# Kernel optimization log

Hardware: AMD Instinct MI355X
Metric: run time of the kernel (lower is better)

The kernel has to match this reference:

```python
import jax, jax.numpy as jnp
import numpy as np

C, H, W = 3, 32, 32
DIM = C * H * W
NUM_CLUSTERS = 4096
BATCH = 8192


def setup_inputs() -> dict:
    key = jax.random.key(0)
    k_x, k_t, k_m = jax.random.split(key, 3)
    x = jax.random.normal(k_x, (BATCH, C, H, W), dtype=jnp.float32)
    t = jax.random.uniform(k_t, (1,), dtype=jnp.float32)
    means = jax.random.normal(k_m, (NUM_CLUSTERS, C, H, W), dtype=jnp.float32)
    # normalize each cluster mean to unit L2 norm over (C,H,W), as in __init__
    norms = jnp.sqrt(jnp.sum(means ** 2, axis=(1, 2, 3), keepdims=True))
    means = means / norms
    standard_dev = jnp.ones((1,), dtype=jnp.float32)  # sqrt(init_variance=1.0)
    return {"x": x, "t": t, "means": means, "standard_dev": standard_dev}


def reference(x, t, means, standard_dev):
    B = x.shape[0]
    x_f = x.reshape(B, -1)                      # [B, D]
    scale = jnp.exp(-t)                         # [1]
    variance = 1.0 - scale ** 2                 # [1]
    variance_t = scale ** 2 * standard_dev ** 2 + variance  # [1]

    sc = means.reshape(means.shape[0], -1) * scale          # [N, D] scaled clusters

    x_sq = jnp.sum(x_f ** 2, axis=-1, keepdims=True)        # [B, 1]
    c_sq = jnp.sum(sc ** 2, axis=-1)[None, :]               # [1, N]
    d2 = jnp.maximum(x_sq + c_sq - 2.0 * (x_f @ sc.T), 0.0)  # [B, N]

    weights = -0.5 * d2 / variance_t                        # [B, N]
    normalized_weights = jax.nn.softmax(weights, axis=-1)   # [B, N]

    cluster_term = normalized_weights @ sc                  # [B, D]

    denoiser_weight = scale ** 2 * standard_dev ** 2 / variance_t  # [1]
    out = denoiser_weight * x_f + (1.0 - denoiser_weight) * cluster_term
    out = out / scale
    return out.reshape(B, C, H, W)
```

## Files before the change

kernel.cpp:

```cpp
#include <hip/hip_runtime.h>
#include <hip/hip_bf16.h>
#include <math.h>
#include <stdint.h>

#define BATCH 8192
#define NCLUST 4096
#define DIM 3072

typedef __bf16 bf16;
typedef __bf16 bf16x4 __attribute__((ext_vector_type(4)));
typedef __bf16 bf16x8 __attribute__((ext_vector_type(8)));
typedef float f32x4 __attribute__((ext_vector_type(4)));

__device__ __forceinline__ void get_scalars(const float* t, const float* sdv,
                                            float& scale, float& vt, float& dw) {
    float s = expf(-t[0]);
    float sd = sdv[0];
    float s2sd2 = s * s * sd * sd;
    float var = 1.0f - s * s;
    scale = s;
    vt = s2sd2 + var;
    dw = s2sd2 / vt;
}

__device__ __forceinline__ void async16(const bf16* g, bf16* l) {
    __builtin_amdgcn_global_load_lds(
        (const __attribute__((address_space(1))) void*)g,
        (__attribute__((address_space(3))) void*)l, 16, 0, 0);
}


__global__ __launch_bounds__(256) void cvt_x_kernel(const float* __restrict__ x,
                                                    bf16* __restrict__ xb, int n4) {
    int i = blockIdx.x * blockDim.x + threadIdx.x;
    if (i >= n4) return;
    float4 v = ((const float4*)x)[i];
    bf16x4 o = {(bf16)v.x, (bf16)v.y, (bf16)v.z, (bf16)v.w};
    ((bf16x4*)xb)[i] = o;
}

__global__ __launch_bounds__(256) void prep_sc_kernel(const float* __restrict__ means,
                                                      const float* __restrict__ t,
                                                      bf16* __restrict__ scb,
                                                      float* __restrict__ c_sq) {
    __shared__ float red[4];
    int row = blockIdx.x, tid = threadIdx.x;
    float scale = expf(-t[0]);
    const float4* m4 = (const float4*)(means + (size_t)row * DIM);
    bf16x4* o4 = (bf16x4*)(scb + (size_t)row * DIM);
    float s = 0.f;
#pragma unroll
    for (int j = 0; j < 3; ++j) {
        float4 v = m4[tid + 256 * j];
        float a = v.x * scale, b = v.y * scale, c = v.z * scale, d = v.w * scale;
        s += a * a + b * b + c * c + d * d;
        bf16x4 o = {(bf16)a, (bf16)b, (bf16)c, (bf16)d};
        o4[tid + 256 * j] = o;
    }
    for (int off = 32; off > 0; off >>= 1) s += __shfl_down(s, off);
    if ((tid & 63) == 0) red[tid >> 6] = s;
    __syncthreads();
    if (tid == 0) c_sq[row] = red[0] + red[1] + red[2] + red[3];
}

__global__ __launch_bounds__(256) void transpose_sc_kernel(const float* __restrict__ means,
                                                           const float* __restrict__ t,
                                                           bf16* __restrict__ scT) {
    __shared__ bf16 tile[64][65];
    float scale = expf(-t[0]);
    int tid = threadIdx.x;
    int tx = tid & 63, ty = tid >> 6;
    int d0 = blockIdx.x * 64, n0 = blockIdx.y * 64;
#pragma unroll
    for (int i = 0; i < 16; ++i) {
        int nr = ty + 4 * i;
        tile[nr][tx] = (bf16)(means[(size_t)(n0 + nr) * DIM + d0 + tx] * scale);
    }
    __syncthreads();
#pragma unroll
    for (int i = 0; i < 16; ++i) {
        int dr = ty + 4 * i;
        scT[(size_t)(d0 + dr) * NCLUST + n0 + tx] = tile[tx][dr];
    }
}


__device__ __forceinline__ void stage2(const bf16* g, size_t ld64, bf16* lds,
                                       int koff, int tid) {
    async16(g + koff, lds + tid * 8);
    async16(g + koff + ld64, lds + (tid + 512) * 8);
}

__global__ __launch_bounds__(512, 2) void gemm256_kernel(
    const bf16* __restrict__ A, const bf16* __restrict__ B,
    int M, int N, int K, int lda,
    const float* __restrict__ t, const float* __restrict__ sdv,
    const float* __restrict__ c_sq, const float* __restrict__ xres,
    float* __restrict__ C, int epi) {
    __shared__ __attribute__((aligned(16))) bf16 As[2][2][128 * 64];
    __shared__ __attribute__((aligned(16))) bf16 Bs[2][2][128 * 64];

    const int tid = threadIdx.x;
    const int lane = tid & 63;
    const int wid = tid >> 6;
    const int wr = wid >> 2;
    const int wc = wid & 3;
    const int lrow = lane & 15;
    const int lq = lane >> 4;
    const int m0 = blockIdx.y * 256, n0 = blockIdx.x * 256;

    const int srow = tid >> 3;
    const int sgc = (tid & 7) ^ (srow & 7);
    const bf16* gA0 = A + (size_t)(m0 + srow) * lda + sgc * 8;
    const bf16* gA1 = gA0 + (size_t)128 * lda;
    const bf16* gB0 = B + (size_t)(n0 + srow) * K + sgc * 8;
    const bf16* gB1 = gB0 + (size_t)128 * K;
    const size_t a64 = (size_t)64 * lda;
    const size_t b64 = (size_t)64 * K;

    const int x7 = lrow & 7;
    const int pos0 = lq ^ x7;
    const int pos1 = (4 + lq) ^ x7;
    const int aoff0 = lrow * 64 + pos0 * 8;
    const int aoff1 = lrow * 64 + pos1 * 8;
    const int brbase = (wc & 1) * 64 + lrow;
    const int boff0 = brbase * 64 + pos0 * 8;
    const int boff1 = brbase * 64 + pos1 * 8;

    f32x4 acc[8][4];
#pragma unroll
    for (int i = 0; i < 8; ++i)
#pragma unroll
        for (int j = 0; j < 4; ++j) acc[i][j] = f32x4{0.f, 0.f, 0.f, 0.f};

    const int NT = K >> 6;

    stage2(gA0, a64, &As[0][0][0], 0, tid);
    stage2(gA1, a64, &As[0][1][0], 0, tid);
    stage2(gB0, b64, &Bs[0][0][0], 0, tid);
    stage2(gB1, b64, &Bs[0][1][0], 0, tid);
    stage2(gB0, b64, &Bs[1][0][0], 64, tid);
    stage2(gA0, a64, &As[1][0][0], 64, tid);
    asm volatile("s_waitcnt vmcnt(4)" ::: "memory");
    __builtin_amdgcn_s_barrier();

    for (int tt = 0; tt < NT; ++tt) {
        const int buf = tt & 1;
        const bf16* Aw = &As[buf][wr][0];
        const bf16* Bw = &Bs[buf][wc >> 1][0];
        bf16x8 a_[4][2], bA[2][2], bB[2][2];

#pragma unroll
        for (int i = 0; i < 4; ++i) {
            a_[i][0] = *(const bf16x8*)(Aw + i * 1024 + aoff0);
            a_[i][1] = *(const bf16x8*)(Aw + i * 1024 + aoff1);
        }
#pragma unroll
        for (int j = 0; j < 2; ++j) {
            bA[j][0] = *(const bf16x8*)(Bw + j * 1024 + boff0);
            bA[j][1] = *(const bf16x8*)(Bw + j * 1024 + boff1);
        }
        if (tt + 1 < NT) stage2(gB1, b64, &Bs[buf ^ 1][1][0], (tt + 1) << 6, tid);
        __builtin_amdgcn_s_barrier();
        asm volatile("s_waitcnt lgkmcnt(0)" ::: "memory");
        __builtin_amdgcn_s_setprio(1);
#pragma unroll
        for (int i = 0; i < 4; ++i)
#pragma unroll
            for (int j = 0; j < 2; ++j) {
                acc[i][j] = __builtin_amdgcn_mfma_f32_16x16x32_bf16(a_[i][0], bA[j][0], acc[i][j], 0, 0, 0);
                acc[i][j] = __builtin_amdgcn_mfma_f32_16x16x32_bf16(a_[i][1], bA[j][1], acc[i][j], 0, 0, 0);
            }
        __builtin_amdgcn_s_setprio(0);
        __builtin_amdgcn_s_barrier();

#pragma unroll
        for (int j = 0; j < 2; ++j) {
            bB[j][0] = *(const bf16x8*)(Bw + (2 + j) * 1024 + boff0);
            bB[j][1] = *(const bf16x8*)(Bw + (2 + j) * 1024 + boff1);
        }
        if (tt + 1 < NT) stage2(gA1, a64, &As[buf ^ 1][1][0], (tt + 1) << 6, tid);
        __builtin_amdgcn_s_barrier();
        asm volatile("s_waitcnt lgkmcnt(0)" ::: "memory");
        __builtin_amdgcn_s_setprio(1);
#pragma unroll
        for (int i = 0; i < 4; ++i)
#pragma unroll
            for (int j = 0; j < 2; ++j) {
                acc[i][2 + j] = __builtin_amdgcn_mfma_f32_16x16x32_bf16(a_[i][0], bB[j][0], acc[i][2 + j], 0, 0, 0);
                acc[i][2 + j] = __builtin_amdgcn_mfma_f32_16x16x32_bf16(a_[i][1], bB[j][1], acc[i][2 + j], 0, 0, 0);
            }
        __builtin_amdgcn_s_setprio(0);
        __builtin_amdgcn_s_barrier();

#pragma unroll
        for (int i = 0; i < 4; ++i) {
            a_[i][0] = *(const bf16x8*)(Aw + (4 + i) * 1024 + aoff0);
            a_[i][1] = *(const bf16x8*)(Aw + (4 + i) * 1024 + aoff1);
        }
        if (tt + 2 < NT) stage2(gB0, b64, &Bs[buf][0][0], (tt + 2) << 6, tid);
        __builtin_amdgcn_s_barrier();
        asm volatile("s_waitcnt lgkmcnt(0)" ::: "memory");
        __builtin_amdgcn_s_setprio(1);
#pragma unroll
        for (int i = 0; i < 4; ++i)
#pragma unroll
            for (int j = 0; j < 2; ++j) {
                acc[4 + i][2 + j] = __builtin_amdgcn_mfma_f32_16x16x32_bf16(a_[i][0], bB[j][0], acc[4 + i][2 + j], 0, 0, 0);
                acc[4 + i][2 + j] = __builtin_amdgcn_mfma_f32_16x16x32_bf16(a_[i][1], bB[j][1], acc[4 + i][2 + j], 0, 0, 0);
            }
        __builtin_amdgcn_s_setprio(0);
        __builtin_amdgcn_s_barrier();

        if (tt + 2 < NT) stage2(gA0, a64, &As[buf][0][0], (tt + 2) << 6, tid);
        __builtin_amdgcn_s_barrier();
        __builtin_amdgcn_s_setprio(1);
#pragma unroll
        for (int i = 0; i < 4; ++i)
#pragma unroll
            for (int j = 0; j < 2; ++j) {
                acc[4 + i][j] = __builtin_amdgcn_mfma_f32_16x16x32_bf16(a_[i][0], bA[j][0], acc[4 + i][j], 0, 0, 0);
                acc[4 + i][j] = __builtin_amdgcn_mfma_f32_16x16x32_bf16(a_[i][1], bA[j][1], acc[4 + i][j], 0, 0, 0);
            }
        __builtin_amdgcn_s_setprio(0);
        if (tt < NT - 2) {
            asm volatile("s_waitcnt vmcnt(4)" ::: "memory");
        } else if (tt == NT - 2) {
            asm volatile("s_waitcnt vmcnt(0)" ::: "memory");
        }
        __builtin_amdgcn_s_barrier();
    }

    float scale, vt, dw;
    get_scalars(t, sdv, scale, vt, dw);

    if (epi == 1) {
        const float inv_vt = 1.0f / vt;
#pragma unroll
        for (int m = 0; m < 8; ++m) {
            int rbase = m0 + wr * 128 + m * 16 + lq * 4;
#pragma unroll
            for (int n = 0; n < 4; ++n) {
                int col = n0 + wc * 64 + n * 16 + lrow;
                float csq = c_sq[col];
#pragma unroll
                for (int r = 0; r < 4; ++r)
                    __builtin_nontemporal_store(
                        (acc[m][n][r] - 0.5f * csq) * inv_vt,
                        &C[(size_t)(rbase + r) * N + col]);
            }
        }
    } else {
        const float inv_scale = 1.0f / scale;
        const float wx = dw * inv_scale;
        const float wcl = (1.0f - dw) * inv_scale;
#pragma unroll
        for (int m = 0; m < 8; ++m) {
            int rbase = m0 + wr * 128 + m * 16 + lq * 4;
#pragma unroll
            for (int n = 0; n < 4; ++n) {
                int col = n0 + wc * 64 + n * 16 + lrow;
#pragma unroll
                for (int r = 0; r < 4; ++r) {
                    size_t idx = (size_t)(rbase + r) * N + col;
                    float xv = __builtin_nontemporal_load(&xres[idx]);
                    __builtin_nontemporal_store(wx * xv + wcl * acc[m][n][r],
                                                &C[idx]);
                }
            }
        }
    }
}

__global__ __launch_bounds__(256) void softmax_kernel(float* __restrict__ S) {
    __shared__ float red[4];
    int b = blockIdx.x, tid = threadIdx.x;
    int lane = tid & 63;
    float* srow = S + (size_t)b * NCLUST;
    const f32x4* s4 = (const f32x4*)srow;
    f32x4 v[4];
#pragma unroll
    for (int j = 0; j < 4; ++j) v[j] = __builtin_nontemporal_load(&s4[tid + 256 * j]);

    float mx = -3.4e38f;
#pragma unroll
    for (int j = 0; j < 4; ++j)
        mx = fmaxf(mx, fmaxf(fmaxf(v[j][0], v[j][1]), fmaxf(v[j][2], v[j][3])));
    for (int off = 32; off > 0; off >>= 1) mx = fmaxf(mx, __shfl_down(mx, off));
    if (lane == 0) red[tid >> 6] = mx;
    __syncthreads();
    mx = fmaxf(fmaxf(red[0], red[1]), fmaxf(red[2], red[3]));
    __syncthreads();

    float e[16];
    float s = 0.f;
#pragma unroll
    for (int j = 0; j < 4; ++j) {
#pragma unroll
        for (int q = 0; q < 4; ++q) {
            e[4 * j + q] = expf(v[j][q] - mx);
            s += e[4 * j + q];
        }
    }
    for (int off = 32; off > 0; off >>= 1) s += __shfl_down(s, off);
    if (lane == 0) red[tid >> 6] = s;
    __syncthreads();
    s = red[0] + red[1] + red[2] + red[3];
    float inv = 1.0f / s;

    bf16x4* p4 = (bf16x4*)srow;
#pragma unroll
    for (int j = 0; j < 4; ++j) {
        bf16x4 o = {(bf16)(e[4 * j + 0] * inv), (bf16)(e[4 * j + 1] * inv),
                    (bf16)(e[4 * j + 2] * inv), (bf16)(e[4 * j + 3] * inv)};
        p4[tid + 256 * j] = o;
    }
}

extern "C" void kernel_launch(void* const* d_in, const int* in_sizes, int n_in,
                              void* d_out, int out_size, void* d_ws, size_t ws_size,
                              hipStream_t stream) {
    const float* x = (const float*)d_in[0];
    const float* t = (const float*)d_in[1];
    const float* means = (const float*)d_in[2];
    const float* sdv = (const float*)d_in[3];
    float* out = (float*)d_out;

    char* ws = (char*)d_ws;
    bf16* xb = (bf16*)ws;
    bf16* scb = (bf16*)(ws + 50331648);
    bf16* scT = (bf16*)(ws + 75497472);
    float* c_sq = (float*)(ws + 100663296);
    float* S = (float*)(ws + 100679680);

    cvt_x_kernel<<<(BATCH * DIM / 4 + 255) / 256, 256, 0, stream>>>(x, xb, BATCH * DIM / 4);
    prep_sc_kernel<<<NCLUST, 256, 0, stream>>>(means, t, scb, c_sq);
    transpose_sc_kernel<<<dim3(DIM / 64, NCLUST / 64), 256, 0, stream>>>(means, t, scT);

    gemm256_kernel<<<dim3(NCLUST / 256, BATCH / 256), 512, 0, stream>>>(
        xb, scb, BATCH, NCLUST, DIM, DIM, t, sdv, c_sq, nullptr, S, 1);

    softmax_kernel<<<BATCH, 256, 0, stream>>>(S);

    gemm256_kernel<<<dim3(DIM / 256, BATCH / 256), 512, 0, stream>>>(
        (const bf16*)S, scT, BATCH, DIM, NCLUST, 2 * NCLUST, t, sdv, nullptr, x, out, 2);
}
```

Baseline: 707.4 us.

## Swizzle block order for L2 locality and deepen full-tile prefetch pipeline

Remaps the flat workgroup index with a stride-8 swizzle so neighbouring workgroups (likely landing on the same XCD) share A/B tiles in L2. Reworks the prefetch schedule so entire next-next K tiles (both halves of A and B) are issued together in the later phases, waiting with vmcnt(8) instead of 4. Adds sched_barriers and reorders MFMAs so independent accumulators interleave rather than back-to-back dependent chains. Risks include wrong swizzle if the grid size is not divisible by 8, and more in-flight loads adding VGPR pressure.

```diff
diff --git a/kernel.cpp b/kernel.cpp
--- a/kernel.cpp
+++ b/kernel.cpp
@@ -107,7 +107,13 @@
     const int wc = wid & 3;
     const int lrow = lane & 15;
     const int lq = lane >> 4;
-    const int m0 = blockIdx.y * 256, n0 = blockIdx.x * 256;
+
+    const int gx = gridDim.x;
+    const int nwg = gx * gridDim.y;
+    const int flat = blockIdx.y * gx + blockIdx.x;
+    const int q8 = nwg >> 3;
+    const int swz = (flat & 7) * q8 + (flat >> 3);
+    const int m0 = (swz / gx) * 256, n0 = (swz % gx) * 256;
 
     const int srow = tid >> 3;
     const int sgc = (tid & 7) ^ (srow & 7);
@@ -140,14 +146,19 @@
     stage2(gB0, b64, &Bs[0][0][0], 0, tid);
     stage2(gB1, b64, &Bs[0][1][0], 0, tid);
     stage2(gB0, b64, &Bs[1][0][0], 64, tid);
+    stage2(gB1, b64, &Bs[1][1][0], 64, tid);
     stage2(gA0, a64, &As[1][0][0], 64, tid);
-    asm volatile("s_waitcnt vmcnt(4)" ::: "memory");
+    stage2(gA1, a64, &As[1][1][0], 64, tid);
+    asm volatile("s_waitcnt vmcnt(8)" ::: "memory");
+    __builtin_amdgcn_sched_barrier(0);
     __builtin_amdgcn_s_barrier();
 
     for (int tt = 0; tt < NT; ++tt) {
         const int buf = tt & 1;
         const bf16* Aw = &As[buf][wr][0];
         const bf16* Bw = &Bs[buf][wc >> 1][0];
+        const int koff2 = (tt + 2) << 6;
+        const bool pf = (tt + 2 < NT);
         bf16x8 a_[4][2], bA[2][2], bB[2][2];
 
 #pragma unroll
@@ -160,17 +171,20 @@
             bA[j][0] = *(const bf16x8*)(Bw + j * 1024 + boff0);
             bA[j][1] = *(const bf16x8*)(Bw + j * 1024 + boff1);
         }
-        if (tt + 1 < NT) stage2(gB1, b64, &Bs[buf ^ 1][1][0], (tt + 1) << 6, tid);
         __builtin_amdgcn_s_barrier();
         asm volatile("s_waitcnt lgkmcnt(0)" ::: "memory");
+        __builtin_amdgcn_sched_barrier(0);
         __builtin_amdgcn_s_setprio(1);
 #pragma unroll
         for (int i = 0; i < 4; ++i)
 #pragma unroll
-            for (int j = 0; j < 2; ++j) {
+            for (int j = 0; j < 2; ++j)
                 acc[i][j] = __builtin_amdgcn_mfma_f32_16x16x32_bf16(a_[i][0], bA[j][0], acc[i][j], 0, 0, 0);
+#pragma unroll
+        for (int i = 0; i < 4; ++i)
+#pragma unroll
+            for (int j = 0; j < 2; ++j)
                 acc[i][j] = __builtin_amdgcn_mfma_f32_16x16x32_bf16(a_[i][1], bA[j][1], acc[i][j], 0, 0, 0);
-            }
         __builtin_amdgcn_s_setprio(0);
         __builtin_amdgcn_s_barrier();
 
@@ -179,17 +193,20 @@
             bB[j][0] = *(const bf16x8*)(Bw + (2 + j) * 1024 + boff0);
             bB[j][1] = *(const bf16x8*)(Bw + (2 + j) * 1024 + boff1);
         }
-        if (tt + 1 < NT) stage2(gA1, a64, &As[buf ^ 1][1][0], (tt + 1) << 6, tid);
         __builtin_amdgcn_s_barrier();
         asm volatile("s_waitcnt lgkmcnt(0)" ::: "memory");
+        __builtin_amdgcn_sched_barrier(0);
         __builtin_amdgcn_s_setprio(1);
 #pragma unroll
         for (int i = 0; i < 4; ++i)
 #pragma unroll
-            for (int j = 0; j < 2; ++j) {
+            for (int j = 0; j < 2; ++j)
                 acc[i][2 + j] = __builtin_amdgcn_mfma_f32_16x16x32_bf16(a_[i][0], bB[j][0], acc[i][2 + j], 0, 0, 0);
+#pragma unroll
+        for (int i = 0; i < 4; ++i)
+#pragma unroll
+            for (int j = 0; j < 2; ++j)
                 acc[i][2 + j] = __builtin_amdgcn_mfma_f32_16x16x32_bf16(a_[i][1], bB[j][1], acc[i][2 + j], 0, 0, 0);
-            }
         __builtin_amdgcn_s_setprio(0);
         __builtin_amdgcn_s_barrier();
 
@@ -198,36 +215,50 @@
             a_[i][0] = *(const bf16x8*)(Aw + (4 + i) * 1024 + aoff0);
             a_[i][1] = *(const bf16x8*)(Aw + (4 + i) * 1024 + aoff1);
         }
-        if (tt + 2 < NT) stage2(gB0, b64, &Bs[buf][0][0], (tt + 2) << 6, tid);
+        if (pf) {
+            stage2(gB0, b64, &Bs[buf][0][0], koff2, tid);
+            stage2(gB1, b64, &Bs[buf][1][0], koff2, tid);
+        }
         __builtin_amdgcn_s_barrier();
         asm volatile("s_waitcnt lgkmcnt(0)" ::: "memory");
+        __builtin_amdgcn_sched_barrier(0);
         __builtin_amdgcn_s_setprio(1);
 #pragma unroll
         for (int i = 0; i < 4; ++i)
 #pragma unroll
-            for (int j = 0; j < 2; ++j) {
+            for (int j = 0; j < 2; ++j)
                 acc[4 + i][2 + j] = __builtin_amdgcn_mfma_f32_16x16x32_bf16(a_[i][0], bB[j][0], acc[4 + i][2 + j], 0, 0, 0);
+#pragma unroll
+        for (int i = 0; i < 4; ++i)
+#pragma unroll
+            for (int j = 0; j < 2; ++j)
                 acc[4 + i][2 + j] = __builtin_amdgcn_mfma_f32_16x16x32_bf16(a_[i][1], bB[j][1], acc[4 + i][2 + j], 0, 0, 0);
-            }
         __builtin_amdgcn_s_setprio(0);
         __builtin_amdgcn_s_barrier();
 
-        if (tt + 2 < NT) stage2(gA0, a64, &As[buf][0][0], (tt + 2) << 6, tid);
+        if (pf) {
+            stage2(gA0, a64, &As[buf][0][0], koff2, tid);
+            stage2(gA1, a64, &As[buf][1][0], koff2, tid);
+        }
         __builtin_amdgcn_s_barrier();
         __builtin_amdgcn_s_setprio(1);
 #pragma unroll
         for (int i = 0; i < 4; ++i)
 #pragma unroll
-            for (int j = 0; j < 2; ++j) {
+            for (int j = 0; j < 2; ++j)
                 acc[4 + i][j] = __builtin_amdgcn_mfma_f32_16x16x32_bf16(a_[i][0], bA[j][0], acc[4 + i][j], 0, 0, 0);
+#pragma unroll
+        for (int i = 0; i < 4; ++i)
+#pragma unroll
+            for (int j = 0; j < 2; ++j)
                 acc[4 + i][j] = __builtin_amdgcn_mfma_f32_16x16x32_bf16(a_[i][1], bA[j][1], acc[4 + i][j], 0, 0, 0);
-            }
         __builtin_amdgcn_s_setprio(0);
         if (tt < NT - 2) {
-            asm volatile("s_waitcnt vmcnt(4)" ::: "memory");
+            asm volatile("s_waitcnt vmcnt(8)" ::: "memory");
         } else if (tt == NT - 2) {
             asm volatile("s_waitcnt vmcnt(0)" ::: "memory");
         }
+        __builtin_amdgcn_sched_barrier(0);
         __builtin_amdgcn_s_barrier();
     }
 
```

Result: slower. 740.4 us (+4.7%).
